# Performance work log

Hardware: AMD Instinct MI355X
Metric: run time of the kernel (lower is better)

Reference implementation:

```python
import jax, jax.numpy as jnp
import numpy as np

ALPHA = 0.8   # dice-score exponent
BETA = 0.2    # class-prob exponent
EPS = 1e-4    # dice denominator epsilon (SparseInst dice_score)


def _hungarian_max(cost):
    """Rectangular linear_sum_assignment(maximize=True) for a numpy (n,m) cost.
    Pads to square, runs the O(s^3) Hungarian algorithm with potentials.
    Returns (rows, cols) of length min(n,m), rows sorted (matches scipy)."""
    n, m = cost.shape
    s = max(n, m)
    c = np.zeros((s, s), dtype=np.float64)
    c[:n, :m] = -cost  # maximize -> minimize
    INF = 1e18
    u = np.zeros(s + 1)
    v = np.zeros(s + 1)
    p = np.zeros(s + 1, dtype=np.int64)
    way = np.zeros(s + 1, dtype=np.int64)
    for i in range(1, s + 1):
        p[0] = i
        j0 = 0
        minv = np.full(s + 1, INF)
        used = np.zeros(s + 1, dtype=bool)
        while True:
            used[j0] = True
            i0 = p[j0]
            cur = c[i0 - 1, :] - u[i0] - v[1:]
            free = ~used[1:]
            upd = free & (cur < minv[1:])
            minv[1:][upd] = cur[upd]
            way[1:][upd] = j0
            cand = np.where(free, minv[1:], INF)
            j1 = int(np.argmin(cand)) + 1
            delta = cand[j1 - 1]
            u[p[used]] += delta
            v[used] -= delta
            minv[~used] -= delta
            j0 = j1
            if p[j0] == 0:
                break
        while j0:
            j1 = way[j0]
            p[j0] = p[j1]
            j0 = j1
    rows, cols = [], []
    for j in range(1, s + 1):
        i = p[j]
        if i - 1 < n and j - 1 < m:
            rows.append(i - 1)
            cols.append(j - 1)
    order = np.argsort(np.asarray(rows))
    return np.asarray(rows)[order], np.asarray(cols)[order]


def _cost_matrix(pred_masks, pred_logits, tgt_masks, tgt_ids):
    B, N, H, W = pred_masks.shape
    T = tgt_masks.shape[0]
    pm = jax.nn.sigmoid(pred_masks.astype(jnp.float32)).reshape(B * N, H * W)
    # bilinear resize (align_corners=False / half-pixel) of GT masks to pred grid
    tm = jax.image.resize(tgt_masks.astype(jnp.float32), (T, H, W), method='linear')
    tm = tm.reshape(T, H * W)
    # dice score: 2<p,t> / (|p|^2 + |t|^2 + eps)   -> (B*N, T)
    num = 2.0 * jnp.einsum('qd,td->qt', pm, tm)
    den = jnp.sum(pm * pm, axis=-1)[:, None] + jnp.sum(tm * tm, axis=-1)[None, :]
    dice = num / (den + EPS)
    prob = jax.nn.sigmoid(pred_logits.astype(jnp.float32)).reshape(B * N, -1)[:, tgt_ids]
    C = dice ** ALPHA * prob ** BETA
    return C.reshape(B, N, T)


_cost_matrix_jit = jax.jit(_cost_matrix)


def setup_inputs() -> dict:
    key = jax.random.key(0)
    k1, k2, k3, k4 = jax.random.split(key, 4)
    B, N, H, W = 16, 100, 128, 128
    T, NC = 320, 80
    return {
        'pred_masks': jax.random.normal(k1, (B, N, H, W), dtype=jnp.float32),
        'pred_logits': jax.random.normal(k2, (B, N, NC), dtype=jnp.float32),
        'tgt_masks': jax.random.uniform(k3, (T, 2 * H, 2 * W), dtype=jnp.float32),
        'tgt_ids': jax.random.randint(k4, (T,), 0, NC, dtype=jnp.int64) if jax.config.jax_enable_x64 else jax.random.randint(k4, (T,), 0, NC, dtype=jnp.int32),
    }


def reference(pred_masks, pred_logits, tgt_masks, tgt_ids):
    B, N = pred_masks.shape[:2]
    T = tgt_masks.shape[0]
    per_img = T // B  # uniform sizes per image (stands in for [len(v['masks'])])
    C = _cost_matrix_jit(pred_masks, pred_logits, tgt_masks, tgt_ids)
    Cn = np.asarray(jax.device_get(C))
    rows, cols = [], []
    for b in range(B):
        r, c = _hungarian_max(Cn[b, :, b * per_img:(b + 1) * per_img])
        rows.append(r)
        cols.append(c)
    rows = jnp.asarray(np.stack(rows), dtype=jnp.int32)  # (B, per_img)
    cols = jnp.asarray(np.stack(cols), dtype=jnp.int32)  # (B, per_img)
    return C, rows, cols
```

## Files before the change

kernel.cpp:

```cpp
#include <hip/hip_runtime.h>
#include <math.h>

#define NB 16
#define NP 100
#define NT 320
#define NCLS 80
#define WO 128
#define HW 16384
#define QT 1600
#define PI 20
#define KSPLIT 8
#define KSLICE 2048
#define KTILES 32
#define SRC_W 256
#define BM 64
#define BN 160
#define CH 16

typedef _Float16 half4v __attribute__((ext_vector_type(4)));
typedef _Float16 half8v __attribute__((ext_vector_type(8)));
typedef float f32x4 __attribute__((ext_vector_type(4)));

#define GLOAD_LDS16(gp, lp) __builtin_amdgcn_global_load_lds(                         \
    (const __attribute__((address_space(1))) void*)(gp),                              \
    (__attribute__((address_space(3))) void*)(lp), 16, 0, 0)

__device__ __forceinline__ float sigf(float x){ return 1.0f/(1.0f+expf(-x)); }
__device__ __forceinline__ float sigfast(float x){ return 1.0f/(1.0f+__expf(-x)); }

__device__ __forceinline__ void mkw128(int i, float* w, int* ix){
  int j0 = 2*i - 1;
  ix[0]=j0; ix[1]=j0+1; ix[2]=j0+2; ix[3]=j0+3;
  w[0]=0.125f; w[1]=0.375f; w[2]=0.375f; w[3]=0.125f;
  if (i == 0){ ix[0]=0; w[0]=0.0f; w[1]=3.0f/7.0f; w[2]=3.0f/7.0f; w[3]=1.0f/7.0f; }
  if (i == 127){ ix[3]=255; w[3]=0.0f; w[0]=1.0f/7.0f; w[1]=3.0f/7.0f; w[2]=3.0f/7.0f; }
}

__global__ __launch_bounds__(256) void k_downsample(const float* __restrict__ tgt,
                                                    _Float16* __restrict__ tm,
                                                    float* __restrict__ tqpart){
  const int blk = blockIdx.x;
  const int t = blk >> 3;
  const int c = blk & 7;
  const int x = threadIdx.x;
  const int oy0 = c * CH;
  const int r0 = 2*oy0 - 1;
  const float* src = tgt + (size_t)t * (SRC_W*SRC_W);
  __shared__ float vbuf[CH][SRC_W];
  __shared__ float wred[4];

  float cc[34];
  #pragma unroll
  for (int li = 0; li < 34; ++li){
    int r = r0 + li; r = r < 0 ? 0 : (r > 255 ? 255 : r);
    cc[li] = src[r*SRC_W + x];
  }
  #pragma unroll
  for (int dy = 0; dy < CH; ++dy){
    int oy = oy0 + dy;
    float w0=0.125f, w1=0.375f, w2=0.375f, w3=0.125f;
    if (oy == 0){ w0=0.0f; w1=3.0f/7.0f; w2=3.0f/7.0f; w3=1.0f/7.0f; }
    if (oy == 127){ w3=0.0f; w0=1.0f/7.0f; w1=3.0f/7.0f; w2=3.0f/7.0f; }
    vbuf[dy][x] = w0*cc[2*dy] + w1*cc[2*dy+1] + w2*cc[2*dy+2] + w3*cc[2*dy+3];
  }
  __syncthreads();

  float ssq = 0.f;
  _Float16* dst = tm + (size_t)t * HW + (size_t)oy0 * WO;
  #pragma unroll
  for (int i = 0; i < 8; ++i){
    int e = x + 256*i;
    int oy = e >> 7;
    int ox = e & 127;
    float w[4]; int ix[4];
    mkw128(ox, w, ix);
    float val = w[0]*vbuf[oy][ix[0]] + w[1]*vbuf[oy][ix[1]]
              + w[2]*vbuf[oy][ix[2]] + w[3]*vbuf[oy][ix[3]];
    dst[oy*WO + ox] = (_Float16)val;
    ssq += val*val;
  }
  for (int off=32; off; off>>=1) ssq += __shfl_xor(ssq, off);
  if ((x & 63) == 0) wred[x >> 6] = ssq;
  __syncthreads();
  if (x == 0) tqpart[c*NT + t] = wred[0]+wred[1]+wred[2]+wred[3];
}

__global__ __launch_bounds__(256) void k_gemm(const float* __restrict__ A,
                                              const _Float16* __restrict__ Bm,
                                              float* __restrict__ part,
                                              float* __restrict__ pqpart){
  __shared__ _Float16 As[BM*64];
  __shared__ _Float16 Bs[BN*64];
  const int tid = threadIdx.x;
  const int lane = tid & 63;
  const int wid = tid >> 6;
  const int q0 = blockIdx.x * BM;
  const int t0 = blockIdx.y * BN;
  const int z  = blockIdx.z;
  const int ks = z * KSLICE;

  const int ar = tid >> 2;
  const int ac = (tid & 3) << 4;
  const float* ap = A + (size_t)(q0 + ar) * HW + ks + ac;

  const int wr = wid >> 1, wc = wid & 1;

  float4 areg[4];
  #pragma unroll
  for (int j = 0; j < 4; ++j) areg[j] = *(const float4*)(ap + j*4);

  f32x4 acc[2][5];
  #pragma unroll
  for (int i = 0; i < 2; ++i)
    #pragma unroll
    for (int n = 0; n < 5; ++n) acc[i][n] = (f32x4){0.f,0.f,0.f,0.f};

  float pqs = 0.f;

  for (int kt = 0; kt < KTILES; ++kt){
    half4v h[4];
    #pragma unroll
    for (int j = 0; j < 4; ++j){
      float4 v = areg[j];
      float s0 = sigfast(v.x), s1 = sigfast(v.y), s2 = sigfast(v.z), s3 = sigfast(v.w);
      pqs += s0*s0 + s1*s1 + s2*s2 + s3*s3;
      half4v hh = { (_Float16)s0, (_Float16)s1, (_Float16)s2, (_Float16)s3 };
      h[j] = hh;
    }
    __syncthreads();
    #pragma unroll
    for (int i = 0; i < 5; ++i){
      int g = wid*320 + i*64 + lane;
      int row = g >> 3;
      int cs = (g & 7) ^ (row & 7);
      const _Float16* gp = Bm + (size_t)(t0 + row) * HW + ks + kt*64 + cs*8;
      GLOAD_LDS16(gp, &Bs[(size_t)g * 8]);
    }
    if (kt + 1 < KTILES){
      #pragma unroll
      for (int j = 0; j < 4; ++j) areg[j] = *(const float4*)(ap + (kt+1)*64 + j*4);
    }
    #pragma unroll
    for (int j = 0; j < 4; ++j){
      int c16 = ((tid & 3) << 1) + (j >> 1);
      int cs = c16 ^ (ar & 7);
      *(half4v*)&As[ar*64 + cs*8 + (j & 1)*4] = h[j];
    }
    __syncthreads();
    #pragma unroll
    for (int s = 0; s < 2; ++s){
      half8v af[2], bf[5];
      int c16 = s*4 + (lane >> 4);
      #pragma unroll
      for (int i = 0; i < 2; ++i){
        int r = wr*32 + i*16 + (lane & 15);
        af[i] = *(const half8v*)&As[r*64 + (c16 ^ (r & 7))*8];
      }
      #pragma unroll
      for (int n = 0; n < 5; ++n){
        int r = wc*80 + n*16 + (lane & 15);
        bf[n] = *(const half8v*)&Bs[r*64 + (c16 ^ (r & 7))*8];
      }
      #pragma unroll
      for (int i = 0; i < 2; ++i)
        #pragma unroll
        for (int n = 0; n < 5; ++n)
          acc[i][n] = __builtin_amdgcn_mfma_f32_16x16x32_f16(af[i], bf[n], acc[i][n], 0, 0, 0);
    }
  }

  float* op = part + (size_t)z * (QT*NT);
  #pragma unroll
  for (int i = 0; i < 2; ++i){
    int qb = q0 + wr*32 + i*16 + (lane >> 4)*4;
    #pragma unroll
    for (int n = 0; n < 5; ++n){
      int t = t0 + wc*80 + n*16 + (lane & 15);
      #pragma unroll
      for (int r = 0; r < 4; ++r)
        op[(size_t)(qb + r)*NT + t] = acc[i][n][r];
    }
  }
  pqs += __shfl_xor(pqs, 1);
  pqs += __shfl_xor(pqs, 2);
  if ((tid & 3) == 0) pqpart[z*QT + q0 + ar] = pqs;
}

__global__ __launch_bounds__(256) void k_cost(const float* __restrict__ part,
                                              const float* __restrict__ pqpart,
                                              const float* __restrict__ tqpart,
                                              const float* __restrict__ logits,
                                              const int* __restrict__ ids,
                                              float* __restrict__ Cout){
  int idx = blockIdx.x * 256 + threadIdx.x;
  int q = idx / NT;
  int t = idx - q * NT;
  float num = 0.f;
  #pragma unroll
  for (int s = 0; s < KSPLIT; ++s) num += part[(size_t)s * (QT*NT) + idx];
  num *= 2.0f;
  float pqv = 0.f;
  #pragma unroll
  for (int s = 0; s < KSPLIT; ++s) pqv += pqpart[s * QT + q];
  float tqv = 0.f;
  #pragma unroll
  for (int s = 0; s < 8; ++s) tqv += tqpart[s * NT + t];
  float den = pqv + tqv + 1e-4f;
  float dice = num / den;
  float prob = sigf(logits[q * NCLS + ids[t]]);
  Cout[idx] = powf(dice, 0.8f) * powf(prob, 0.2f);
}

__global__ __launch_bounds__(64) void k_hung(const float* __restrict__ C,
                                             float* __restrict__ rows_out,
                                             float* __restrict__ cols_out){
  const int b = blockIdx.x;
  const int lane = threadIdx.x;
  __shared__ float negC[PI*NP];
  __shared__ double u[PI+1];
  __shared__ int p[NP+1];
  __shared__ int way[NP+1];
  for (int e = lane; e < PI*NP; e += 64){
    int i = e / NP, j = e - i*NP;
    negC[e] = -C[(size_t)(b*NP + j)*NT + (b*PI + i)];
  }
  if (lane <= PI) u[lane] = 0.0;
  for (int j = lane; j <= NP; j += 64){ p[j] = 0; way[j] = 0; }
  __syncthreads();
  const int jA = lane + 1;
  const int jB = lane + 65;
  const bool hasB = (jB <= NP);
  double vA = 0.0, vB = 0.0;
  const double INFD = 1e18;
  for (int i = 1; i <= PI; ++i){
    if (lane == 0) p[0] = i;
    __syncthreads();
    double mvA = INFD, mvB = INFD;
    bool usA = false, usB = false;
    int j0 = 0;
    int jbrk = 0;
    while (true){
      if (jA == j0) usA = true;
      if (hasB && jB == j0) usB = true;
      int i0 = p[j0];
      double ui0 = u[i0];
      double candA = INFD, candB = INFD;
      if (!usA){
        double cur = (double)negC[(i0-1)*NP + (jA-1)] - ui0 - vA;
        if (cur < mvA){ mvA = cur; way[jA] = j0; }
        candA = mvA;
      }
      if (hasB && !usB){
        double cur = (double)negC[(i0-1)*NP + (jB-1)] - ui0 - vB;
        if (cur < mvB){ mvB = cur; way[jB] = j0; }
        candB = mvB;
      }
      double bv; int bj;
      if (candB < candA){ bv = candB; bj = jB; } else { bv = candA; bj = jA; }
      for (int off = 32; off; off >>= 1){
        double ov = __shfl_xor(bv, off);
        int oj = __shfl_xor(bj, off);
        if (ov < bv || (ov == bv && oj < bj)){ bv = ov; bj = oj; }
      }
      const double delta = bv;
      if (usA){ int pj = p[jA]; u[pj] += delta; vA -= delta; }
      else mvA -= delta;
      if (hasB){
        if (usB){ int pj = p[jB]; u[pj] += delta; vB -= delta; }
        else mvB -= delta;
      }
      if (lane == 0) u[p[0]] += delta;
      __syncthreads();
      j0 = bj;
      if (p[j0] == 0){ jbrk = j0; break; }
    }
    __syncthreads();
    if (lane == 0){
      int j0a = jbrk;
      while (j0a){
        int jp = way[j0a];
        p[j0a] = p[jp];
        j0a = jp;
      }
    }
    __syncthreads();
  }
  if (lane == 0){
    int cnt = 0;
    for (int j = 1; j <= NP; ++j){
      int pi = p[j];
      if (pi != 0){
        rows_out[b*PI + cnt] = (float)(j - 1);
        cols_out[b*PI + cnt] = (float)(pi - 1);
        ++cnt;
      }
    }
  }
}

extern "C" void kernel_launch(void* const* d_in, const int* in_sizes, int n_in,
                              void* d_out, int out_size, void* d_ws, size_t ws_size,
                              hipStream_t stream){
  const float* pred_masks  = (const float*)d_in[0];
  const float* pred_logits = (const float*)d_in[1];
  const float* tgt_masks   = (const float*)d_in[2];
  const int*   tgt_ids     = (const int*)d_in[3];
  float* out = (float*)d_out;
  char* ws = (char*)d_ws;
  _Float16* Th  = (_Float16*)ws;
  float* tqpart = (float*)(ws + (size_t)NT*HW*2);
  float* pqpart = (float*)(ws + (size_t)NT*HW*2 + 16384);
  float* part   = (float*)(ws + (size_t)NT*HW*2 + 16384 + 65536);

  k_downsample<<<NT*8, 256, 0, stream>>>(tgt_masks, Th, tqpart);
  dim3 g(QT/BM, NT/BN, KSPLIT);
  k_gemm<<<g, 256, 0, stream>>>(pred_masks, Th, part, pqpart);
  k_cost<<<(QT*NT)/256, 256, 0, stream>>>(part, pqpart, tqpart, pred_logits, tgt_ids, out);
  k_hung<<<NB, 64, 0, stream>>>(out, out + (size_t)QT*NT, out + (size_t)QT*NT + NT);
}
```

Measured before the change: 124.8 us.

## Restructure GEMM tiling to cover all targets per block with double-buffered LDS

```diff
diff --git a/kernel.cpp b/kernel.cpp
--- a/kernel.cpp
+++ b/kernel.cpp
@@ -11,12 +11,14 @@
 #define PI 20
 #define KSPLIT 8
 #define KSLICE 2048
-#define KTILES 32
+#define BK 32
+#define KTILES 64
 #define SRC_W 256
-#define BM 64
-#define BN 160
+#define BM 32
+#define BN 320
 #define CH 16
 
+typedef _Float16 half2v __attribute__((ext_vector_type(2)));
 typedef _Float16 half4v __attribute__((ext_vector_type(4)));
 typedef _Float16 half8v __attribute__((ext_vector_type(8)));
 typedef float f32x4 __attribute__((ext_vector_type(4)));
@@ -24,6 +26,8 @@
 #define GLOAD_LDS16(gp, lp) __builtin_amdgcn_global_load_lds(                         \
     (const __attribute__((address_space(1))) void*)(gp),                              \
     (__attribute__((address_space(3))) void*)(lp), 16, 0, 0)
+
+#define SWZ(r) (((r) & 3) ^ (((r) >> 2) & 3))
 
 __device__ __forceinline__ float sigf(float x){ return 1.0f/(1.0f+expf(-x)); }
 __device__ __forceinline__ float sigfast(float x){ return 1.0f/(1.0f+__expf(-x)); }
@@ -85,105 +89,103 @@
   if (x == 0) tqpart[c*NT + t] = wred[0]+wred[1]+wred[2]+wred[3];
 }
 
-__global__ __launch_bounds__(256) void k_gemm(const float* __restrict__ A,
+__global__ __launch_bounds__(512) void k_gemm(const float* __restrict__ A,
                                               const _Float16* __restrict__ Bm,
                                               float* __restrict__ part,
                                               float* __restrict__ pqpart){
-  __shared__ _Float16 As[BM*64];
-  __shared__ _Float16 Bs[BN*64];
+  __shared__ _Float16 As[2][BM*BK];
+  __shared__ _Float16 Bs[2][BN*BK];
   const int tid = threadIdx.x;
   const int lane = tid & 63;
   const int wid = tid >> 6;
-  const int q0 = blockIdx.x * BM;
-  const int t0 = blockIdx.y * BN;
-  const int z  = blockIdx.z;
+  const int wr = wid & 1;
+  const int wc = wid >> 1;
+  const int id = blockIdx.x;
+  const int z = id & 7;
+  const int q0 = (id >> 3) * BM;
   const int ks = z * KSLICE;
 
-  const int ar = tid >> 2;
-  const int ac = (tid & 3) << 4;
-  const float* ap = A + (size_t)(q0 + ar) * HW + ks + ac;
-
-  const int wr = wid >> 1, wc = wid & 1;
-
-  float4 areg[4];
-  #pragma unroll
-  for (int j = 0; j < 4; ++j) areg[j] = *(const float4*)(ap + j*4);
-
-  f32x4 acc[2][5];
-  #pragma unroll
-  for (int i = 0; i < 2; ++i)
-    #pragma unroll
-    for (int n = 0; n < 5; ++n) acc[i][n] = (f32x4){0.f,0.f,0.f,0.f};
-
+  const int ar = tid >> 4;
+  const int acg = tid & 15;
+  const float* ap = A + (size_t)(q0 + ar) * HW + ks + acg*2;
+  const int awoff = ar*BK + ((acg >> 2) ^ SWZ(ar))*8 + (acg & 3)*2;
+
+  f32x4 acc[5];
+  #pragma unroll
+  for (int n = 0; n < 5; ++n) acc[n] = (f32x4){0.f,0.f,0.f,0.f};
   float pqs = 0.f;
 
+  #pragma unroll
+  for (int i = 0; i < 3; ++i){
+    int g = i*512 + tid;
+    if (g < 1280){
+      int row = g >> 2, slot = g & 3;
+      const _Float16* gp = Bm + (size_t)row*HW + ks + (slot ^ SWZ(row))*8;
+      GLOAD_LDS16(gp, &Bs[0][(size_t)g*8]);
+    }
+  }
+  {
+    float2 a0 = *(const float2*)ap;
+    float s0 = sigfast(a0.x), s1 = sigfast(a0.y);
+    pqs += s0*s0 + s1*s1;
+    half2v hh = { (_Float16)s0, (_Float16)s1 };
+    *(half2v*)&As[0][awoff] = hh;
+  }
+  __syncthreads();
+
   for (int kt = 0; kt < KTILES; ++kt){
-    half4v h[4];
-    #pragma unroll
-    for (int j = 0; j < 4; ++j){
-      float4 v = areg[j];
-      float s0 = sigfast(v.x), s1 = sigfast(v.y), s2 = sigfast(v.z), s3 = sigfast(v.w);
-      pqs += s0*s0 + s1*s1 + s2*s2 + s3*s3;
-      half4v hh = { (_Float16)s0, (_Float16)s1, (_Float16)s2, (_Float16)s3 };
-      h[j] = hh;
-    }
-    __syncthreads();
-    #pragma unroll
-    for (int i = 0; i < 5; ++i){
-      int g = wid*320 + i*64 + lane;
-      int row = g >> 3;
-      int cs = (g & 7) ^ (row & 7);
-      const _Float16* gp = Bm + (size_t)(t0 + row) * HW + ks + kt*64 + cs*8;
-      GLOAD_LDS16(gp, &Bs[(size_t)g * 8]);
-    }
+    const int cur = kt & 1, nxt = cur ^ 1;
+    float2 a;
     if (kt + 1 < KTILES){
       #pragma unroll
-      for (int j = 0; j < 4; ++j) areg[j] = *(const float4*)(ap + (kt+1)*64 + j*4);
-    }
-    #pragma unroll
-    for (int j = 0; j < 4; ++j){
-      int c16 = ((tid & 3) << 1) + (j >> 1);
-      int cs = c16 ^ (ar & 7);
-      *(half4v*)&As[ar*64 + cs*8 + (j & 1)*4] = h[j];
-    }
-    __syncthreads();
-    #pragma unroll
-    for (int s = 0; s < 2; ++s){
-      half8v af[2], bf[5];
-      int c16 = s*4 + (lane >> 4);
-      #pragma unroll
-      for (int i = 0; i < 2; ++i){
-        int r = wr*32 + i*16 + (lane & 15);
-        af[i] = *(const half8v*)&As[r*64 + (c16 ^ (r & 7))*8];
-      }
-      #pragma unroll
-      for (int n = 0; n < 5; ++n){
-        int r = wc*80 + n*16 + (lane & 15);
-        bf[n] = *(const half8v*)&Bs[r*64 + (c16 ^ (r & 7))*8];
-      }
-      #pragma unroll
-      for (int i = 0; i < 2; ++i)
-        #pragma unroll
-        for (int n = 0; n < 5; ++n)
-          acc[i][n] = __builtin_amdgcn_mfma_f32_16x16x32_f16(af[i], bf[n], acc[i][n], 0, 0, 0);
-    }
-  }
-
-  float* op = part + (size_t)z * (QT*NT);
-  #pragma unroll
-  for (int i = 0; i < 2; ++i){
-    int qb = q0 + wr*32 + i*16 + (lane >> 4)*4;
+      for (int i = 0; i < 3; ++i){
+        int g = i*512 + tid;
+        if (g < 1280){
+          int row = g >> 2, slot = g & 3;
+          const _Float16* gp = Bm + (size_t)row*HW + ks + (kt+1)*BK + (slot ^ SWZ(row))*8;
+          GLOAD_LDS16(gp, &Bs[nxt][(size_t)g*8]);
+        }
+      }
+      a = *(const float2*)(ap + (kt+1)*BK);
+    }
+    half8v af, bf[5];
+    {
+      int r = wr*16 + (lane & 15);
+      af = *(const half8v*)&As[cur][r*BK + (((lane>>4) ^ SWZ(r)))*8];
+    }
     #pragma unroll
     for (int n = 0; n < 5; ++n){
-      int t = t0 + wc*80 + n*16 + (lane & 15);
+      int r = wc*80 + n*16 + (lane & 15);
+      bf[n] = *(const half8v*)&Bs[cur][r*BK + (((lane>>4) ^ SWZ(r)))*8];
+    }
+    #pragma unroll
+    for (int n = 0; n < 5; ++n)
+      acc[n] = __builtin_amdgcn_mfma_f32_16x16x32_f16(af, bf[n], acc[n], 0, 0, 0);
+    if (kt + 1 < KTILES){
+      float s0 = sigfast(a.x), s1 = sigfast(a.y);
+      pqs += s0*s0 + s1*s1;
+      half2v hh = { (_Float16)s0, (_Float16)s1 };
+      *(half2v*)&As[nxt][awoff] = hh;
+    }
+    __syncthreads();
+  }
+
+  float* op = part + (size_t)z * (QT*NT);
+  {
+    int qb = q0 + wr*16 + (lane >> 4)*4;
+    #pragma unroll
+    for (int n = 0; n < 5; ++n){
+      int t = wc*80 + n*16 + (lane & 15);
       #pragma unroll
       for (int r = 0; r < 4; ++r)
-        op[(size_t)(qb + r)*NT + t] = acc[i][n][r];
+        op[(size_t)(qb + r)*NT + t] = acc[n][r];
     }
   }
   pqs += __shfl_xor(pqs, 1);
   pqs += __shfl_xor(pqs, 2);
-  if ((tid & 3) == 0) pqpart[z*QT + q0 + ar] = pqs;
+  pqs += __shfl_xor(pqs, 4);
+  pqs += __shfl_xor(pqs, 8);
+  if ((tid & 15) == 0) pqpart[z*QT + q0 + ar] = pqs;
 }
 
 __global__ __launch_bounds__(256) void k_cost(const float* __restrict__ part,
@@ -313,8 +315,7 @@
   float* part   = (float*)(ws + (size_t)NT*HW*2 + 16384 + 65536);
 
   k_downsample<<<NT*8, 256, 0, stream>>>(tgt_masks, Th, tqpart);
-  dim3 g(QT/BM, NT/BN, KSPLIT);
-  k_gemm<<<g, 256, 0, stream>>>(pred_masks, Th, part, pqpart);
+  k_gemm<<<50*KSPLIT, 512, 0, stream>>>(pred_masks, Th, part, pqpart);
   k_cost<<<(QT*NT)/256, 256, 0, stream>>>(part, pqpart, tqpart, pred_logits, tgt_ids, out);
   k_hung<<<NB, 64, 0, stream>>>(out, out + (size_t)QT*NT, out + (size_t)QT*NT + NT);
 }
```

Result: slower. 138.2 us (+10.8%).

## Retile GEMM to cover all targets per block with triple-buffered LDS pipeline

Applied to the files above, without the earlier changes.

```diff
diff --git a/kernel.cpp b/kernel.cpp
--- a/kernel.cpp
+++ b/kernel.cpp
@@ -11,10 +11,11 @@
 #define PI 20
 #define KSPLIT 8
 #define KSLICE 2048
-#define KTILES 32
+#define BK 32
+#define KTILES 64
 #define SRC_W 256
-#define BM 64
-#define BN 160
+#define BM 32
+#define BN 320
 #define CH 16
 
 typedef _Float16 half4v __attribute__((ext_vector_type(4)));
@@ -24,6 +25,8 @@
 #define GLOAD_LDS16(gp, lp) __builtin_amdgcn_global_load_lds(                         \
     (const __attribute__((address_space(1))) void*)(gp),                              \
     (__attribute__((address_space(3))) void*)(lp), 16, 0, 0)
+
+#define SWZ(r) (((r) & 3) ^ (((r) >> 2) & 3))
 
 __device__ __forceinline__ float sigf(float x){ return 1.0f/(1.0f+expf(-x)); }
 __device__ __forceinline__ float sigfast(float x){ return 1.0f/(1.0f+__expf(-x)); }
@@ -89,93 +92,104 @@
                                               const _Float16* __restrict__ Bm,
                                               float* __restrict__ part,
                                               float* __restrict__ pqpart){
-  __shared__ _Float16 As[BM*64];
-  __shared__ _Float16 Bs[BN*64];
+  __shared__ _Float16 Bs[3][BN*BK];
+  __shared__ _Float16 As[2][BM*BK];
   const int tid = threadIdx.x;
   const int lane = tid & 63;
   const int wid = tid >> 6;
-  const int q0 = blockIdx.x * BM;
-  const int t0 = blockIdx.y * BN;
-  const int z  = blockIdx.z;
+  const int id = blockIdx.x;
+  const int z = id & 7;
+  const int q0 = (id >> 3) * BM;
   const int ks = z * KSLICE;
 
-  const int ar = tid >> 2;
-  const int ac = (tid & 3) << 4;
-  const float* ap = A + (size_t)(q0 + ar) * HW + ks + ac;
-
-  const int wr = wid >> 1, wc = wid & 1;
-
-  float4 areg[4];
-  #pragma unroll
-  for (int j = 0; j < 4; ++j) areg[j] = *(const float4*)(ap + j*4);
+  const int ar = tid >> 3;
+  const int acg = tid & 7;
+  const float* ap = A + (size_t)(q0 + ar) * HW + ks + acg*4;
+  const int awoff = ar*BK + ((acg >> 1) ^ SWZ(ar))*8 + (acg & 1)*4;
 
   f32x4 acc[2][5];
   #pragma unroll
   for (int i = 0; i < 2; ++i)
     #pragma unroll
     for (int n = 0; n < 5; ++n) acc[i][n] = (f32x4){0.f,0.f,0.f,0.f};
-
   float pqs = 0.f;
 
+  {
+    float4 a0 = *(const float4*)ap;
+    float s0 = sigfast(a0.x), s1 = sigfast(a0.y), s2 = sigfast(a0.z), s3 = sigfast(a0.w);
+    pqs += s0*s0 + s1*s1 + s2*s2 + s3*s3;
+    half4v hh = { (_Float16)s0, (_Float16)s1, (_Float16)s2, (_Float16)s3 };
+    *(half4v*)&As[0][awoff] = hh;
+  }
+  #pragma unroll
+  for (int i = 0; i < 5; ++i){
+    int g = i*256 + tid;
+    int row = g >> 2, slot = g & 3;
+    GLOAD_LDS16(Bm + (size_t)row*HW + ks + (slot ^ SWZ(row))*8, &Bs[0][(size_t)g*8]);
+  }
+  #pragma unroll
+  for (int i = 0; i < 5; ++i){
+    int g = i*256 + tid;
+    int row = g >> 2, slot = g & 3;
+    GLOAD_LDS16(Bm + (size_t)row*HW + ks + BK + (slot ^ SWZ(row))*8, &Bs[1][(size_t)g*8]);
+  }
+  float4 aCur = *(const float4*)(ap + BK);
+  asm volatile("s_waitcnt vmcnt(5) lgkmcnt(0)" ::: "memory");
+  __builtin_amdgcn_s_barrier();
+
   for (int kt = 0; kt < KTILES; ++kt){
-    half4v h[4];
-    #pragma unroll
-    for (int j = 0; j < 4; ++j){
-      float4 v = areg[j];
-      float s0 = sigfast(v.x), s1 = sigfast(v.y), s2 = sigfast(v.z), s3 = sigfast(v.w);
+    float4 aNext;
+    if (kt + 2 < KTILES){
+      aNext = *(const float4*)(ap + (kt+2)*BK);
+      const _Float16* bbase = Bm + (size_t)(ks + (kt+2)*BK);
+      _Float16* lds = &Bs[(kt+2)%3][0];
+      #pragma unroll
+      for (int i = 0; i < 5; ++i){
+        int g = i*256 + tid;
+        int row = g >> 2, slot = g & 3;
+        GLOAD_LDS16(bbase + (size_t)row*HW + (slot ^ SWZ(row))*8, lds + (size_t)g*8);
+      }
+    }
+    const _Float16* bb = &Bs[kt%3][0];
+    const _Float16* aa = &As[kt&1][0];
+    half8v af[2], bf[5];
+    #pragma unroll
+    for (int i = 0; i < 2; ++i){
+      int r = i*16 + (lane & 15);
+      af[i] = *(const half8v*)&aa[r*BK + (((lane>>4) ^ SWZ(r)))*8];
+    }
+    #pragma unroll
+    for (int n = 0; n < 5; ++n){
+      int r = wid*80 + n*16 + (lane & 15);
+      bf[n] = *(const half8v*)&bb[r*BK + (((lane>>4) ^ SWZ(r)))*8];
+    }
+    #pragma unroll
+    for (int i = 0; i < 2; ++i)
+      #pragma unroll
+      for (int n = 0; n < 5; ++n)
+        acc[i][n] = __builtin_amdgcn_mfma_f32_16x16x32_f16(af[i], bf[n], acc[i][n], 0, 0, 0);
+    if (kt + 1 < KTILES){
+      float s0 = sigfast(aCur.x), s1 = sigfast(aCur.y), s2 = sigfast(aCur.z), s3 = sigfast(aCur.w);
       pqs += s0*s0 + s1*s1 + s2*s2 + s3*s3;
       half4v hh = { (_Float16)s0, (_Float16)s1, (_Float16)s2, (_Float16)s3 };
-      h[j] = hh;
-    }
-    __syncthreads();
-    #pragma unroll
-    for (int i = 0; i < 5; ++i){
-      int g = wid*320 + i*64 + lane;
-      int row = g >> 3;
-      int cs = (g & 7) ^ (row & 7);
-      const _Float16* gp = Bm + (size_t)(t0 + row) * HW + ks + kt*64 + cs*8;
-      GLOAD_LDS16(gp, &Bs[(size_t)g * 8]);
-    }
-    if (kt + 1 < KTILES){
-      #pragma unroll
-      for (int j = 0; j < 4; ++j) areg[j] = *(const float4*)(ap + (kt+1)*64 + j*4);
-    }
-    #pragma unroll
-    for (int j = 0; j < 4; ++j){
-      int c16 = ((tid & 3) << 1) + (j >> 1);
-      int cs = c16 ^ (ar & 7);
-      *(half4v*)&As[ar*64 + cs*8 + (j & 1)*4] = h[j];
-    }
-    __syncthreads();
-    #pragma unroll
-    for (int s = 0; s < 2; ++s){
-      half8v af[2], bf[5];
-      int c16 = s*4 + (lane >> 4);
-      #pragma unroll
-      for (int i = 0; i < 2; ++i){
-        int r = wr*32 + i*16 + (lane & 15);
-        af[i] = *(const half8v*)&As[r*64 + (c16 ^ (r & 7))*8];
-      }
-      #pragma unroll
-      for (int n = 0; n < 5; ++n){
-        int r = wc*80 + n*16 + (lane & 15);
-        bf[n] = *(const half8v*)&Bs[r*64 + (c16 ^ (r & 7))*8];
-      }
-      #pragma unroll
-      for (int i = 0; i < 2; ++i)
-        #pragma unroll
-        for (int n = 0; n < 5; ++n)
-          acc[i][n] = __builtin_amdgcn_mfma_f32_16x16x32_f16(af[i], bf[n], acc[i][n], 0, 0, 0);
-    }
+      *(half4v*)&As[(kt+1)&1][awoff] = hh;
+      aCur = aNext;
+    }
+    if (kt + 2 < KTILES){
+      asm volatile("s_waitcnt vmcnt(6) lgkmcnt(0)" ::: "memory");
+    } else {
+      asm volatile("s_waitcnt vmcnt(0) lgkmcnt(0)" ::: "memory");
+    }
+    __builtin_amdgcn_s_barrier();
   }
 
   float* op = part + (size_t)z * (QT*NT);
   #pragma unroll
   for (int i = 0; i < 2; ++i){
-    int qb = q0 + wr*32 + i*16 + (lane >> 4)*4;
+    int qb = q0 + i*16 + (lane >> 4)*4;
     #pragma unroll
     for (int n = 0; n < 5; ++n){
-      int t = t0 + wc*80 + n*16 + (lane & 15);
+      int t = wid*80 + n*16 + (lane & 15);
       #pragma unroll
       for (int r = 0; r < 4; ++r)
         op[(size_t)(qb + r)*NT + t] = acc[i][n][r];
@@ -183,7 +197,8 @@
   }
   pqs += __shfl_xor(pqs, 1);
   pqs += __shfl_xor(pqs, 2);
-  if ((tid & 3) == 0) pqpart[z*QT + q0 + ar] = pqs;
+  pqs += __shfl_xor(pqs, 4);
+  if ((tid & 7) == 0) pqpart[z*QT + q0 + ar] = pqs;
 }
 
 __global__ __launch_bounds__(256) void k_cost(const float* __restrict__ part,
@@ -313,8 +328,7 @@
   float* part   = (float*)(ws + (size_t)NT*HW*2 + 16384 + 65536);
 
   k_downsample<<<NT*8, 256, 0, stream>>>(tgt_masks, Th, tqpart);
-  dim3 g(QT/BM, NT/BN, KSPLIT);
-  k_gemm<<<g, 256, 0, stream>>>(pred_masks, Th, part, pqpart);
+  k_gemm<<<50*KSPLIT, 256, 0, stream>>>(pred_masks, Th, part, pqpart);
   k_cost<<<(QT*NT)/256, 256, 0, stream>>>(part, pqpart, tqpart, pred_logits, tgt_ids, out);
   k_hung<<<NB, 64, 0, stream>>>(out, out + (size_t)QT*NT, out + (size_t)QT*NT + NT);
 }
```

Result: slower. 132.5 us (+6.2%).
